# Kernel optimization log

Measured on AMD Instinct MI355X. Metric: run time of the kernel, lower is better.

## Reference

```python
import math
import jax, jax.numpy as jnp
import numpy as np

N_EMBD = 1024
N_HEAD = 16
HEAD_DIM = N_EMBD // N_HEAD


def setup_inputs() -> dict:
    key = jax.random.key(0)
    ks = jax.random.split(key, 5)
    B, S = 4, 2048
    x = jax.random.normal(ks[0], (B, S, 2, N_EMBD), dtype=jnp.float32)
    Wt = jax.random.normal(ks[1], (N_EMBD, 3 * N_EMBD), dtype=jnp.float32) * 0.02
    Ws = jax.random.normal(ks[2], (N_EMBD, 2 * N_EMBD), dtype=jnp.float32) * 0.02
    Wo = jax.random.normal(ks[3], (N_EMBD, N_EMBD), dtype=jnp.float32) * 0.02
    lam_ts = jnp.ones((1,), dtype=jnp.float32)
    lam_st = jnp.ones((1,), dtype=jnp.float32)
    lam_ss = jnp.ones((1,), dtype=jnp.float32)
    return {"x": x, "Wt": Wt, "Ws": Ws, "Wo": Wo,
            "lam_ts": lam_ts, "lam_st": lam_st, "lam_ss": lam_ss}


def _heads(t, B, S):
    # [B,S,E] -> [B,H,S,D]
    return t.reshape(B, S, N_HEAD, HEAD_DIM).transpose(0, 2, 1, 3)


def reference(x, Wt, Ws, Wo, lam_ts, lam_st, lam_ss):
    B, S, _, E = x.shape
    xt = x[:, :, 0, :]  # text stream [B,S,E]
    xs = x[:, :, 1, :]  # spatial stream [B,S,E]

    qt, kt, vt = jnp.split(xt @ Wt, 3, axis=-1)
    qs, ks = jnp.split(xs @ Ws, 2, axis=-1)
    qt, kt, vt = _heads(qt, B, S), _heads(kt, B, S), _heads(vt, B, S)
    qs, ks = _heads(qs, B, S), _heads(ks, B, S)

    scale = 1.0 / math.sqrt(HEAD_DIM)
    att = (jnp.einsum('bhqd,bhkd->bhqk', qt, kt)
           + lam_ts[0] * jnp.einsum('bhqd,bhkd->bhqk', qt, ks)
           + lam_st[0] * jnp.einsum('bhqd,bhkd->bhqk', qs, kt)
           + lam_ss[0] * jnp.einsum('bhqd,bhkd->bhqk', qs, ks)) * scale
    att = jax.nn.softmax(att, axis=-1)

    y = jnp.einsum('bhqk,bhkd->bhqd', att, vt)  # [B,H,S,D]
    y = y.transpose(0, 2, 1, 3).reshape(B, S, E)
    y = y @ Wo
    # concat text output with untouched spatial stream -> [B,S,2,E]
    return jnp.concatenate([y[:, :, None, :], xs[:, :, None, :]], axis=2)
```

## Files before the change

kernel.cpp:

```cpp
#include <hip/hip_runtime.h>

typedef short  short8  __attribute__((ext_vector_type(8)));
typedef float  f32x4   __attribute__((ext_vector_type(4)));
typedef ushort u16x4   __attribute__((ext_vector_type(4)));

__device__ __forceinline__ float bf2f(ushort u) {
  union { unsigned u; float f; } v; v.u = ((unsigned)u) << 16; return v.f;
}
__device__ __forceinline__ ushort f2bf(float f) {
  union { float f; unsigned u; } v; v.f = f;
  unsigned r = v.u + 0x7FFF + ((v.u >> 16) & 1);
  return (ushort)(r >> 16);
}
__device__ __forceinline__ float exp2_fast(float x) {
  float r; asm("v_exp_f32 %0, %1" : "=v"(r) : "v"(x)); return r;
}

__device__ __forceinline__ void gload16(const ushort* g, ushort* l) {
  __builtin_amdgcn_global_load_lds(
      (__attribute__((address_space(1))) void*)(void*)(const_cast<ushort*>(g)),
      (__attribute__((address_space(3))) void*)(void*)l, 16, 0, 0);
}


__global__ __launch_bounds__(256) void prep_x(const float* __restrict__ x,
                                              ushort* __restrict__ xt,
                                              ushort* __restrict__ xs,
                                              float* __restrict__ out) {
  size_t i = ((size_t)blockIdx.x * 256 + threadIdx.x) * 4;
  size_t m = i >> 10, e = i & 1023;
  f32x4 a = *(const f32x4*)&x[m * 2048 + e];
  f32x4 b = *(const f32x4*)&x[m * 2048 + 1024 + e];
  u16x4 ta, tb;
#pragma unroll
  for (int j = 0; j < 4; ++j) { ta[j] = f2bf(a[j]); tb[j] = f2bf(b[j]); }
  *(u16x4*)&xt[i] = ta;
  *(u16x4*)&xs[i] = tb;
  *(f32x4*)&out[m * 2048 + 1024 + e] = b;
}

__global__ __launch_bounds__(256) void transpose_w(const float* __restrict__ W,
                                                   ushort* __restrict__ Wt,
                                                   int K, int N) {
  __shared__ float tile[32][33];
  int n0 = blockIdx.x * 32, k0 = blockIdx.y * 32;
  int tx = threadIdx.x & 31, ty = threadIdx.x >> 5;
#pragma unroll
  for (int i = 0; i < 32; i += 8)
    tile[ty + i][tx] = W[(size_t)(k0 + ty + i) * N + n0 + tx];
  __syncthreads();
#pragma unroll
  for (int i = 0; i < 32; i += 8)
    Wt[(size_t)(n0 + ty + i) * K + k0 + tx] = f2bf(tile[tx][ty + i]);
}

template <int F32OUT>
__global__ __launch_bounds__(256) void gemm_bt(const ushort* __restrict__ A,
                                               const ushort* __restrict__ Bt,
                                               ushort* __restrict__ Cb,
                                               float* __restrict__ Cf,
                                               int N, int ldc) {
  const int K = 1024;
  __shared__ ushort sA[128 * 32];
  __shared__ ushort sB[128 * 32];
  const int tid = threadIdx.x;
  const int wave = tid >> 6, lane = tid & 63;
  const int wr = wave >> 1, wc = wave & 1;
  const int l15 = lane & 15, l4 = lane >> 4;
  const int m0 = blockIdx.y * 128, n0 = blockIdx.x * 128;

  f32x4 acc[4][4];
  const f32x4 z = {0.f, 0.f, 0.f, 0.f};
#pragma unroll
  for (int a = 0; a < 4; ++a)
#pragma unroll
    for (int b = 0; b < 4; ++b) acc[a][b] = z;

  for (int k0 = 0; k0 < K; k0 += 32) {
#pragma unroll
    for (int j = 0; j < 2; ++j) {
      int cb = j * 256 + wave * 64;
      int c = cb + lane;
      int row = c >> 2, cc = c & 3;
      gload16(&A [(size_t)(m0 + row) * K + k0 + cc * 8], &sA[cb * 8]);
      gload16(&Bt[(size_t)(n0 + row) * K + k0 + cc * 8], &sB[cb * 8]);
    }
    __syncthreads();
    short8 af[4], bfr[4];
#pragma unroll
    for (int i = 0; i < 4; ++i) {
      af[i]  = *(const short8*)&sA[(wr * 64 + i * 16 + l15) * 32 + l4 * 8];
      bfr[i] = *(const short8*)&sB[(wc * 64 + i * 16 + l15) * 32 + l4 * 8];
    }
#pragma unroll
    for (int mi = 0; mi < 4; ++mi)
#pragma unroll
      for (int ni = 0; ni < 4; ++ni)
        acc[mi][ni] = __builtin_amdgcn_mfma_f32_16x16x32_bf16(af[mi], bfr[ni], acc[mi][ni], 0, 0, 0);
    __syncthreads();
  }

#pragma unroll
  for (int mi = 0; mi < 4; ++mi)
#pragma unroll
    for (int ni = 0; ni < 4; ++ni) {
      int row = m0 + wr * 64 + mi * 16 + l4 * 4;
      int col = n0 + wc * 64 + ni * 16 + l15;
#pragma unroll
      for (int r = 0; r < 4; ++r) {
        if constexpr (F32OUT) Cf[(size_t)(row + r) * ldc + col] = acc[mi][ni][r];
        else                  Cb[(size_t)(row + r) * ldc + col] = f2bf(acc[mi][ni][r]);
      }
    }
}

__global__ __launch_bounds__(256) void scatter_qk(const ushort* __restrict__ Ct,
                                                  const ushort* __restrict__ Cs,
                                                  ushort* __restrict__ Qb,
                                                  ushort* __restrict__ Kb,
                                                  const float* plts, const float* plst,
                                                  const float* plss) {
  int tid = blockIdx.x * 256 + threadIdx.x;
  int m = tid >> 7, u = tid & 127;
  int b = m >> 11, s = m & 2047;
  int h = u >> 3, din = (u & 7) * 8;
  float lts = plts[0], lst = plst[0], lss = plss[0];
  const float scale = 0.125f * 1.44269504f;
  short8 qt = *(const short8*)&Ct[(size_t)m * 3072 + u * 8];
  short8 kt = *(const short8*)&Ct[(size_t)m * 3072 + 1024 + u * 8];
  short8 qs = *(const short8*)&Cs[(size_t)m * 2048 + u * 8];
  short8 ks = *(const short8*)&Cs[(size_t)m * 2048 + 1024 + u * 8];
  short8 oqt, oqs, k1, k2;
#pragma unroll
  for (int j = 0; j < 8; ++j) {
    float fqt = bf2f((ushort)qt[j]), fqs = bf2f((ushort)qs[j]);
    float fkt = bf2f((ushort)kt[j]), fks = bf2f((ushort)ks[j]);
    oqt[j] = (short)f2bf(fqt * scale);
    oqs[j] = (short)f2bf(fqs * scale);
    k1[j]  = (short)f2bf(fkt + lts * fks);
    k2[j]  = (short)f2bf(lst * fkt + lss * fks);
  }
  size_t base = ((size_t)(b * 16 + h) * 2048 + s) * 128;
  *(short8*)&Qb[base + din]      = oqt;
  *(short8*)&Qb[base + 64 + din] = oqs;
  int c1 = ((u & 7) ^ (s & 7)) * 8;
  *(short8*)&Kb[base + c1]      = k1;
  *(short8*)&Kb[base + 64 + c1] = k2;
}

__global__ __launch_bounds__(256) void transpose_v(const ushort* __restrict__ Ct,
                                                   ushort* __restrict__ Vt) {
  int bh = blockIdx.y; int s0 = blockIdx.x * 64;
  int b = bh >> 4, h = bh & 15;
  __shared__ ushort t[64][72];
  int tid = threadIdx.x;
#pragma unroll
  for (int j = 0; j < 2; ++j) {
    int c = j * 256 + tid;
    int srow = c >> 3, cc = c & 7;
    *(short8*)&t[srow][cc * 8] =
        *(const short8*)&Ct[(size_t)(b * 2048 + s0 + srow) * 3072 + 2048 + h * 64 + cc * 8];
  }
  __syncthreads();
#pragma unroll
  for (int j = 0; j < 2; ++j) {
    int c = j * 256 + tid;
    int drow = c >> 3, cc = c & 7;
    short8 v;
#pragma unroll
    for (int k = 0; k < 8; ++k) v[k] = t[cc * 8 + k][drow];
    *(short8*)&Vt[((size_t)bh * 64 + drow) * 2048 + s0 + ((cc ^ (drow & 7)) * 8)] = v;
  }
}

__global__ __launch_bounds__(256) void attn_kernel(const ushort* __restrict__ Q,
                                                   const ushort* __restrict__ Kg,
                                                   const ushort* __restrict__ Vg,
                                                   ushort* __restrict__ Y) {
  const int id   = blockIdx.x;
  const int virt = (id & 7) * 128 + (id >> 3);
  const int bh = virt >> 4;
  const int q0 = (virt & 15) * 128;
  const int tid = threadIdx.x;
  const int wave = tid >> 6, lane = tid & 63;
  const int l15 = lane & 15, l4 = lane >> 4;
  const size_t qkb = (size_t)bh * 2048 * 128;
  const size_t vb  = (size_t)bh * 64 * 2048;

  __shared__ ushort sKV[2 * 64 * 128 + 2 * 64 * 64];
  ushort* const sK0 = sKV;
  ushort* const sV0 = sKV + 2 * 64 * 128;

  auto stage = [&](int kv0, int bufi) {
    ushort* dK = sK0 + bufi * (64 * 128);
    ushort* dV = sV0 + bufi * (64 * 64);
#pragma unroll
    for (int j = 0; j < 4; ++j) {
      int base = j * 256 + wave * 64;
      int c = base + lane, row = c >> 4, cc = c & 15;
      gload16(&Kg[qkb + (size_t)(kv0 + row) * 128 + cc * 8], &dK[base * 8]);
    }
#pragma unroll
    for (int j = 0; j < 2; ++j) {
      int base = j * 256 + wave * 64;
      int c = base + lane, row = c >> 3, cc = c & 7;
      gload16(&Vg[vb + (size_t)row * 2048 + kv0 + cc * 8], &dV[base * 8]);
    }
  };

  short8 qf[2][4];
#pragma unroll
  for (int qi = 0; qi < 2; ++qi) {
    int qrow = q0 + wave * 32 + qi * 16 + l15;
#pragma unroll
    for (int kk = 0; kk < 4; ++kk)
      qf[qi][kk] = *(const short8*)&Q[qkb + (size_t)qrow * 128 + kk * 32 + l4 * 8];
  }
  const f32x4 z = {0.f, 0.f, 0.f, 0.f};
  f32x4 accO[2][4] = {{z, z, z, z}, {z, z, z, z}};
  float mrow[2] = {-3.0e38f, -3.0e38f}, lrow[2] = {0.f, 0.f};

  stage(0, 0);
  __syncthreads();

  for (int t = 0; t < 32; ++t) {
    const int cur = t & 1;
    if (t < 31) stage((t + 1) * 64, cur ^ 1);
    const ushort* cK = sK0 + cur * (64 * 128);
    const ushort* cV = sV0 + cur * (64 * 64);

    f32x4 sc[2][4] = {{z, z, z, z}, {z, z, z, z}};
    __builtin_amdgcn_s_setprio(1);
#pragma unroll
    for (int kk = 0; kk < 4; ++kk)
#pragma unroll
      for (int kb = 0; kb < 4; ++kb) {
        int row = kb * 16 + l15;
        const short8 kf = *(const short8*)&cK[row * 128 + (((kk * 4 + l4) ^ (row & 7)) * 8)];
        sc[0][kb] = __builtin_amdgcn_mfma_f32_16x16x32_bf16(kf, qf[0][kk], sc[0][kb], 0, 0, 0);
        sc[1][kb] = __builtin_amdgcn_mfma_f32_16x16x32_bf16(kf, qf[1][kk], sc[1][kb], 0, 0, 0);
      }
    __builtin_amdgcn_s_setprio(0);

    union { uint u4[4]; short8 s8; } pa[2][2];
#pragma unroll
    for (int qi = 0; qi < 2; ++qi) {
      float mx = sc[qi][0][0];
#pragma unroll
      for (int kb = 0; kb < 4; ++kb)
#pragma unroll
        for (int r = 0; r < 4; ++r) mx = fmaxf(mx, sc[qi][kb][r]);
      mx = fmaxf(mx, __shfl_xor(mx, 16));
      mx = fmaxf(mx, __shfl_xor(mx, 32));

      if (__any(mx > mrow[qi] + 8.f)) {
        float mnew = fmaxf(mrow[qi], mx);
        float corr = exp2_fast(mrow[qi] - mnew);
        mrow[qi] = mnew;
        lrow[qi] *= corr;
#pragma unroll
        for (int r = 0; r < 4; ++r) {
          float cq = __shfl(corr, l4 * 4 + r);
#pragma unroll
          for (int nf = 0; nf < 4; ++nf) accO[qi][nf][r] *= cq;
        }
      }

      float ps = 0.f;
#pragma unroll
      for (int kb = 0; kb < 4; ++kb)
#pragma unroll
        for (int r = 0; r < 4; ++r) {
          float e = exp2_fast(sc[qi][kb][r] - mrow[qi]);
          sc[qi][kb][r] = e; ps += e;
        }
      lrow[qi] += ps;

      uint u00, u01, u10, u11, u20, u21, u30, u31;
#define CVTPK(d, a, b) asm("v_cvt_pk_bf16_f32 %0, %1, %2" : "=v"(d) : "v"(a), "v"(b))
      CVTPK(u00, sc[qi][0][0], sc[qi][0][1]); CVTPK(u01, sc[qi][0][2], sc[qi][0][3]);
      CVTPK(u10, sc[qi][1][0], sc[qi][1][1]); CVTPK(u11, sc[qi][1][2], sc[qi][1][3]);
      CVTPK(u20, sc[qi][2][0], sc[qi][2][1]); CVTPK(u21, sc[qi][2][2], sc[qi][2][3]);
      CVTPK(u30, sc[qi][3][0], sc[qi][3][1]); CVTPK(u31, sc[qi][3][2], sc[qi][3][3]);
#undef CVTPK
      asm volatile("v_permlane32_swap_b32 %0, %1" : "+v"(u00), "+v"(u10));
      asm volatile("v_permlane32_swap_b32 %0, %1" : "+v"(u01), "+v"(u11));
      asm volatile("v_permlane32_swap_b32 %0, %1" : "+v"(u20), "+v"(u30));
      asm volatile("v_permlane32_swap_b32 %0, %1" : "+v"(u21), "+v"(u31));
      asm volatile("v_permlane16_swap_b32 %0, %1" : "+v"(u00), "+v"(u10));
      asm volatile("v_permlane16_swap_b32 %0, %1" : "+v"(u01), "+v"(u11));
      asm volatile("v_permlane16_swap_b32 %0, %1" : "+v"(u20), "+v"(u30));
      asm volatile("v_permlane16_swap_b32 %0, %1" : "+v"(u21), "+v"(u31));
      pa[qi][0].u4[0] = u00; pa[qi][0].u4[1] = u01; pa[qi][0].u4[2] = u10; pa[qi][0].u4[3] = u11;
      pa[qi][1].u4[0] = u20; pa[qi][1].u4[1] = u21; pa[qi][1].u4[2] = u30; pa[qi][1].u4[3] = u31;
    }

    __builtin_amdgcn_s_setprio(1);
#pragma unroll
    for (int nf = 0; nf < 4; ++nf) {
      int d = nf * 16 + l15;
      const short8 vf0 = *(const short8*)&cV[d * 64 + ((l4 ^ (d & 7)) * 8)];
      const short8 vf1 = *(const short8*)&cV[d * 64 + (((4 + l4) ^ (d & 7)) * 8)];
      accO[0][nf] = __builtin_amdgcn_mfma_f32_16x16x32_bf16(pa[0][0].s8, vf0, accO[0][nf], 0, 0, 0);
      accO[1][nf] = __builtin_amdgcn_mfma_f32_16x16x32_bf16(pa[1][0].s8, vf0, accO[1][nf], 0, 0, 0);
      accO[0][nf] = __builtin_amdgcn_mfma_f32_16x16x32_bf16(pa[0][1].s8, vf1, accO[0][nf], 0, 0, 0);
      accO[1][nf] = __builtin_amdgcn_mfma_f32_16x16x32_bf16(pa[1][1].s8, vf1, accO[1][nf], 0, 0, 0);
    }
    __builtin_amdgcn_s_setprio(0);

    __syncthreads();
  }

  int b = bh >> 4, hh = bh & 15;
#pragma unroll
  for (int qi = 0; qi < 2; ++qi) {
    float ls = lrow[qi] + __shfl_xor(lrow[qi], 16);
    ls += __shfl_xor(ls, 32);
    float linv = 1.f / ls;
#pragma unroll
    for (int r = 0; r < 4; ++r) {
      float lq = __shfl(linv, l4 * 4 + r);
      int q = q0 + wave * 32 + qi * 16 + l4 * 4 + r;
#pragma unroll
      for (int nf = 0; nf < 4; ++nf)
        Y[((size_t)b * 2048 + q) * 1024 + hh * 64 + nf * 16 + l15] =
            f2bf(accO[qi][nf][r] * lq);
    }
  }
}

extern "C" void kernel_launch(void* const* d_in, const int* in_sizes, int n_in,
                              void* d_out, int out_size, void* d_ws, size_t ws_size,
                              hipStream_t stream) {
  const float* x   = (const float*)d_in[0];
  const float* Wt  = (const float*)d_in[1];
  const float* Ws  = (const float*)d_in[2];
  const float* Wo  = (const float*)d_in[3];
  const float* lts = (const float*)d_in[4];
  const float* lst = (const float*)d_in[5];
  const float* lss = (const float*)d_in[6];
  float* out = (float*)d_out;
  char* ws = (char*)d_ws;

  ushort* xt    = (ushort*)(ws + 0);
  ushort* xs    = (ushort*)(ws + 16777216);
  ushort* Qbuf  = (ushort*)(ws + 0);
  ushort* Wt_bt = (ushort*)(ws + 33554432);
  ushort* Ws_bt = (ushort*)(ws + 39845888);
  ushort* Wo_bt = (ushort*)(ws + 44040192);
  ushort* Ct    = (ushort*)(ws + 46137344);
  ushort* Ybuf  = (ushort*)(ws + 46137344);
  ushort* Cs    = (ushort*)(ws + 96468992);
  ushort* Kbuf  = (ushort*)(ws + 130023424);
  ushort* Vtbuf = (ushort*)(ws + 163577856);
  (void)in_sizes; (void)n_in; (void)out_size; (void)ws_size;

  prep_x<<<8192, 256, 0, stream>>>(x, xt, xs, out);
  transpose_w<<<dim3(96, 32), 256, 0, stream>>>(Wt, Wt_bt, 1024, 3072);
  transpose_w<<<dim3(64, 32), 256, 0, stream>>>(Ws, Ws_bt, 1024, 2048);
  transpose_w<<<dim3(32, 32), 256, 0, stream>>>(Wo, Wo_bt, 1024, 1024);
  gemm_bt<0><<<dim3(24, 64), 256, 0, stream>>>(xt, Wt_bt, Ct, nullptr, 3072, 3072);
  gemm_bt<0><<<dim3(16, 64), 256, 0, stream>>>(xs, Ws_bt, Cs, nullptr, 2048, 2048);
  scatter_qk<<<4096, 256, 0, stream>>>(Ct, Cs, Qbuf, Kbuf, lts, lst, lss);
  transpose_v<<<dim3(32, 64), 256, 0, stream>>>(Ct, Vtbuf);
  attn_kernel<<<1024, 256, 0, stream>>>(Qbuf, Kbuf, Vtbuf, Ybuf);
  gemm_bt<1><<<dim3(8, 64), 256, 0, stream>>>(Ybuf, Wo_bt, nullptr, out, 1024, 2048);
}
```

Baseline: 335.4 us.

## Replace double-buffered K/V staging with single buffers and split-phase prefetch

Shared memory for K and V drops from two buffers each to one, which cuts LDS use per block roughly in half and may allow more resident blocks per CU. The next K tile is loaded after the softmax (overlapping the PV MFMAs), and the next V tile after the end-of-iteration barrier. This adds a barrier per iteration and leaves less time to hide load latency, since the next QK step waits on K fetched during PV only.

```diff
diff --git a/kernel.cpp b/kernel.cpp
--- a/kernel.cpp
+++ b/kernel.cpp
@@ -187,24 +187,23 @@
   const size_t qkb = (size_t)bh * 2048 * 128;
   const size_t vb  = (size_t)bh * 64 * 2048;
 
-  __shared__ ushort sKV[2 * 64 * 128 + 2 * 64 * 64];
-  ushort* const sK0 = sKV;
-  ushort* const sV0 = sKV + 2 * 64 * 128;
-
-  auto stage = [&](int kv0, int bufi) {
-    ushort* dK = sK0 + bufi * (64 * 128);
-    ushort* dV = sV0 + bufi * (64 * 64);
+  __shared__ ushort sK[64 * 128];
+  __shared__ ushort sV[64 * 64];
+
+  auto stageK = [&](int kv0) {
 #pragma unroll
     for (int j = 0; j < 4; ++j) {
       int base = j * 256 + wave * 64;
       int c = base + lane, row = c >> 4, cc = c & 15;
-      gload16(&Kg[qkb + (size_t)(kv0 + row) * 128 + cc * 8], &dK[base * 8]);
-    }
+      gload16(&Kg[qkb + (size_t)(kv0 + row) * 128 + cc * 8], &sK[base * 8]);
+    }
+  };
+  auto stageV = [&](int kv0) {
 #pragma unroll
     for (int j = 0; j < 2; ++j) {
       int base = j * 256 + wave * 64;
       int c = base + lane, row = c >> 3, cc = c & 7;
-      gload16(&Vg[vb + (size_t)row * 2048 + kv0 + cc * 8], &dV[base * 8]);
+      gload16(&Vg[vb + (size_t)row * 2048 + kv0 + cc * 8], &sV[base * 8]);
     }
   };
 
@@ -220,15 +219,11 @@
   f32x4 accO[2][4] = {{z, z, z, z}, {z, z, z, z}};
   float mrow[2] = {-3.0e38f, -3.0e38f}, lrow[2] = {0.f, 0.f};
 
-  stage(0, 0);
+  stageK(0);
+  stageV(0);
   __syncthreads();
 
   for (int t = 0; t < 32; ++t) {
-    const int cur = t & 1;
-    if (t < 31) stage((t + 1) * 64, cur ^ 1);
-    const ushort* cK = sK0 + cur * (64 * 128);
-    const ushort* cV = sV0 + cur * (64 * 64);
-
     f32x4 sc[2][4] = {{z, z, z, z}, {z, z, z, z}};
     __builtin_amdgcn_s_setprio(1);
 #pragma unroll
@@ -236,7 +231,7 @@
 #pragma unroll
       for (int kb = 0; kb < 4; ++kb) {
         int row = kb * 16 + l15;
-        const short8 kf = *(const short8*)&cK[row * 128 + (((kk * 4 + l4) ^ (row & 7)) * 8)];
+        const short8 kf = *(const short8*)&sK[row * 128 + (((kk * 4 + l4) ^ (row & 7)) * 8)];
         sc[0][kb] = __builtin_amdgcn_mfma_f32_16x16x32_bf16(kf, qf[0][kk], sc[0][kb], 0, 0, 0);
         sc[1][kb] = __builtin_amdgcn_mfma_f32_16x16x32_bf16(kf, qf[1][kk], sc[1][kb], 0, 0, 0);
       }
@@ -295,12 +290,15 @@
       pa[qi][1].u4[0] = u20; pa[qi][1].u4[1] = u21; pa[qi][1].u4[2] = u30; pa[qi][1].u4[3] = u31;
     }
 
+    __syncthreads();
+    if (t < 31) stageK((t + 1) * 64);
+
     __builtin_amdgcn_s_setprio(1);
 #pragma unroll
     for (int nf = 0; nf < 4; ++nf) {
       int d = nf * 16 + l15;
-      const short8 vf0 = *(const short8*)&cV[d * 64 + ((l4 ^ (d & 7)) * 8)];
-      const short8 vf1 = *(const short8*)&cV[d * 64 + (((4 + l4) ^ (d & 7)) * 8)];
+      const short8 vf0 = *(const short8*)&sV[d * 64 + ((l4 ^ (d & 7)) * 8)];
+      const short8 vf1 = *(const short8*)&sV[d * 64 + (((4 + l4) ^ (d & 7)) * 8)];
       accO[0][nf] = __builtin_amdgcn_mfma_f32_16x16x32_bf16(pa[0][0].s8, vf0, accO[0][nf], 0, 0, 0);
       accO[1][nf] = __builtin_amdgcn_mfma_f32_16x16x32_bf16(pa[1][0].s8, vf0, accO[1][nf], 0, 0, 0);
       accO[0][nf] = __builtin_amdgcn_mfma_f32_16x16x32_bf16(pa[0][1].s8, vf1, accO[0][nf], 0, 0, 0);
@@ -309,6 +307,7 @@
     __builtin_amdgcn_s_setprio(0);
 
     __syncthreads();
+    if (t < 31) stageV((t + 1) * 64);
   }
 
   int b = bh >> 4, hh = bh & 15;
```

Measured after the change: 341.3 us. Within noise of the previous version (+1.8%).

## Fuse Q/K scatter and lambda mixing into projection GEMM epilogues

Applied to the files above, without the earlier changes.

Removes the scatter_qk kernel. The text-stream GEMM now writes Q heads directly into the head-major Q buffer and keeps only K/V in a smaller row-major buffer. The spatial GEMM writes Qs into the buffer and computes the lambda-mixed swizzled K from the stored Kt in its epilogue. The softmax scale on Q is folded into the transposed weights. This saves one kernel launch and a full read/write pass over the Q/K intermediates, but the epilogue now does scalar 2-byte scattered stores instead of vectorized 16-byte ones.

```diff
diff --git a/kernel.cpp b/kernel.cpp
--- a/kernel.cpp
+++ b/kernel.cpp
@@ -41,7 +41,8 @@
 
 __global__ __launch_bounds__(256) void transpose_w(const float* __restrict__ W,
                                                    ushort* __restrict__ Wt,
-                                                   int K, int N) {
+                                                   int K, int N, int nq,
+                                                   float qscale) {
   __shared__ float tile[32][33];
   int n0 = blockIdx.x * 32, k0 = blockIdx.y * 32;
   int tx = threadIdx.x & 31, ty = threadIdx.x >> 5;
@@ -50,16 +51,25 @@
     tile[ty + i][tx] = W[(size_t)(k0 + ty + i) * N + n0 + tx];
   __syncthreads();
 #pragma unroll
-  for (int i = 0; i < 32; i += 8)
-    Wt[(size_t)(n0 + ty + i) * K + k0 + tx] = f2bf(tile[tx][ty + i]);
-}
-
-template <int F32OUT>
+  for (int i = 0; i < 32; i += 8) {
+    int n = n0 + ty + i;
+    float v = tile[tx][ty + i];
+    if (n < nq) v *= qscale;
+    Wt[(size_t)n * K + k0 + tx] = f2bf(v);
+  }
+}
+
+template <int EPI>
 __global__ __launch_bounds__(256) void gemm_bt(const ushort* __restrict__ A,
                                                const ushort* __restrict__ Bt,
-                                               ushort* __restrict__ Cb,
-                                               float* __restrict__ Cf,
-                                               int N, int ldc) {
+                                               int N,
+                                               ushort* __restrict__ o1,
+                                               ushort* __restrict__ o2,
+                                               const ushort* __restrict__ ct2,
+                                               float* __restrict__ of,
+                                               const float* plts,
+                                               const float* plst,
+                                               const float* plss) {
   const int K = 1024;
   __shared__ ushort sA[128 * 32];
   __shared__ ushort sB[128 * 32];
@@ -100,55 +110,60 @@
     __syncthreads();
   }
 
+  float lts = 0.f, lst = 0.f, lss = 0.f;
+  if constexpr (EPI == 2) { lts = plts[0]; lst = plst[0]; lss = plss[0]; }
+
 #pragma unroll
   for (int mi = 0; mi < 4; ++mi)
 #pragma unroll
     for (int ni = 0; ni < 4; ++ni) {
-      int row = m0 + wr * 64 + mi * 16 + l4 * 4;
-      int col = n0 + wc * 64 + ni * 16 + l15;
-#pragma unroll
-      for (int r = 0; r < 4; ++r) {
-        if constexpr (F32OUT) Cf[(size_t)(row + r) * ldc + col] = acc[mi][ni][r];
-        else                  Cb[(size_t)(row + r) * ldc + col] = f2bf(acc[mi][ni][r]);
+      int rowb = m0 + wr * 64 + mi * 16 + l4 * 4;
+      int col  = n0 + wc * 64 + ni * 16 + l15;
+      if constexpr (EPI == 0) {
+#pragma unroll
+        for (int r = 0; r < 4; ++r)
+          of[(size_t)(rowb + r) * 2048 + col] = acc[mi][ni][r];
+      } else if constexpr (EPI == 1) {
+        if (col < 1024) {
+          int h = col >> 6, d = col & 63;
+#pragma unroll
+          for (int r = 0; r < 4; ++r) {
+            int s = rowb + r, b = s >> 11, ss = s & 2047;
+            o1[((size_t)(b * 16 + h) * 2048 + ss) * 128 + d] = f2bf(acc[mi][ni][r]);
+          }
+        } else {
+#pragma unroll
+          for (int r = 0; r < 4; ++r)
+            o2[(size_t)(rowb + r) * 2048 + (col - 1024)] = f2bf(acc[mi][ni][r]);
+        }
+      } else {
+        if (col < 1024) {
+          int h = col >> 6, d = col & 63;
+#pragma unroll
+          for (int r = 0; r < 4; ++r) {
+            int s = rowb + r, b = s >> 11, ss = s & 2047;
+            o1[((size_t)(b * 16 + h) * 2048 + ss) * 128 + 64 + d] = f2bf(acc[mi][ni][r]);
+          }
+        } else {
+          int d64 = col - 1024, h = d64 >> 6, d = d64 & 63;
+#pragma unroll
+          for (int r = 0; r < 4; ++r) {
+            int s = rowb + r, b = s >> 11, ss = s & 2047;
+            float kt = bf2f(ct2[(size_t)s * 2048 + d64]);
+            float ks = acc[mi][ni][r];
+            float k1 = kt + lts * ks;
+            float k2 = lst * kt + lss * ks;
+            size_t base = ((size_t)(b * 16 + h) * 2048 + ss) * 128;
+            int off = ((((d >> 3) ^ (ss & 7)) << 3)) + (d & 7);
+            o2[base + off]      = f2bf(k1);
+            o2[base + 64 + off] = f2bf(k2);
+          }
+        }
       }
     }
 }
 
-__global__ __launch_bounds__(256) void scatter_qk(const ushort* __restrict__ Ct,
-                                                  const ushort* __restrict__ Cs,
-                                                  ushort* __restrict__ Qb,
-                                                  ushort* __restrict__ Kb,
-                                                  const float* plts, const float* plst,
-                                                  const float* plss) {
-  int tid = blockIdx.x * 256 + threadIdx.x;
-  int m = tid >> 7, u = tid & 127;
-  int b = m >> 11, s = m & 2047;
-  int h = u >> 3, din = (u & 7) * 8;
-  float lts = plts[0], lst = plst[0], lss = plss[0];
-  const float scale = 0.125f * 1.44269504f;
-  short8 qt = *(const short8*)&Ct[(size_t)m * 3072 + u * 8];
-  short8 kt = *(const short8*)&Ct[(size_t)m * 3072 + 1024 + u * 8];
-  short8 qs = *(const short8*)&Cs[(size_t)m * 2048 + u * 8];
-  short8 ks = *(const short8*)&Cs[(size_t)m * 2048 + 1024 + u * 8];
-  short8 oqt, oqs, k1, k2;
-#pragma unroll
-  for (int j = 0; j < 8; ++j) {
-    float fqt = bf2f((ushort)qt[j]), fqs = bf2f((ushort)qs[j]);
-    float fkt = bf2f((ushort)kt[j]), fks = bf2f((ushort)ks[j]);
-    oqt[j] = (short)f2bf(fqt * scale);
-    oqs[j] = (short)f2bf(fqs * scale);
-    k1[j]  = (short)f2bf(fkt + lts * fks);
-    k2[j]  = (short)f2bf(lst * fkt + lss * fks);
-  }
-  size_t base = ((size_t)(b * 16 + h) * 2048 + s) * 128;
-  *(short8*)&Qb[base + din]      = oqt;
-  *(short8*)&Qb[base + 64 + din] = oqs;
-  int c1 = ((u & 7) ^ (s & 7)) * 8;
-  *(short8*)&Kb[base + c1]      = k1;
-  *(short8*)&Kb[base + 64 + c1] = k2;
-}
-
-__global__ __launch_bounds__(256) void transpose_v(const ushort* __restrict__ Ct,
+__global__ __launch_bounds__(256) void transpose_v(const ushort* __restrict__ Ct2,
                                                    ushort* __restrict__ Vt) {
   int bh = blockIdx.y; int s0 = blockIdx.x * 64;
   int b = bh >> 4, h = bh & 15;
@@ -159,7 +174,7 @@
     int c = j * 256 + tid;
     int srow = c >> 3, cc = c & 7;
     *(short8*)&t[srow][cc * 8] =
-        *(const short8*)&Ct[(size_t)(b * 2048 + s0 + srow) * 3072 + 2048 + h * 64 + cc * 8];
+        *(const short8*)&Ct2[(size_t)(b * 2048 + s0 + srow) * 2048 + 1024 + h * 64 + cc * 8];
   }
   __syncthreads();
 #pragma unroll
@@ -344,25 +359,28 @@
 
   ushort* xt    = (ushort*)(ws + 0);
   ushort* xs    = (ushort*)(ws + 16777216);
-  ushort* Qbuf  = (ushort*)(ws + 0);
   ushort* Wt_bt = (ushort*)(ws + 33554432);
   ushort* Ws_bt = (ushort*)(ws + 39845888);
   ushort* Wo_bt = (ushort*)(ws + 44040192);
-  ushort* Ct    = (ushort*)(ws + 46137344);
-  ushort* Ybuf  = (ushort*)(ws + 46137344);
-  ushort* Cs    = (ushort*)(ws + 96468992);
-  ushort* Kbuf  = (ushort*)(ws + 130023424);
-  ushort* Vtbuf = (ushort*)(ws + 163577856);
+  ushort* Ct2   = (ushort*)(ws + 46137344);
+  ushort* Qbuf  = (ushort*)(ws + 79691776);
+  ushort* Kbuf  = (ushort*)(ws + 113246208);
+  ushort* Vtbuf = (ushort*)(ws + 146800640);
+  ushort* Ybuf  = (ushort*)(ws + 163577856);
   (void)in_sizes; (void)n_in; (void)out_size; (void)ws_size;
 
+  const float qscale = 0.125f * 1.44269504f;
+
   prep_x<<<8192, 256, 0, stream>>>(x, xt, xs, out);
-  transpose_w<<<dim3(96, 32), 256, 0, stream>>>(Wt, Wt_bt, 1024, 3072);
-  transpose_w<<<dim3(64, 32), 256, 0, stream>>>(Ws, Ws_bt, 1024, 2048);
-  transpose_w<<<dim3(32, 32), 256, 0, stream>>>(Wo, Wo_bt, 1024, 1024);
-  gemm_bt<0><<<dim3(24, 64), 256, 0, stream>>>(xt, Wt_bt, Ct, nullptr, 3072, 3072);
-  gemm_bt<0><<<dim3(16, 64), 256, 0, stream>>>(xs, Ws_bt, Cs, nullptr, 2048, 2048);
-  scatter_qk<<<4096, 256, 0, stream>>>(Ct, Cs, Qbuf, Kbuf, lts, lst, lss);
-  transpose_v<<<dim3(32, 64), 256, 0, stream>>>(Ct, Vtbuf);
+  transpose_w<<<dim3(96, 32), 256, 0, stream>>>(Wt, Wt_bt, 1024, 3072, 1024, qscale);
+  transpose_w<<<dim3(64, 32), 256, 0, stream>>>(Ws, Ws_bt, 1024, 2048, 1024, qscale);
+  transpose_w<<<dim3(32, 32), 256, 0, stream>>>(Wo, Wo_bt, 1024, 1024, 0, 1.f);
+  gemm_bt<1><<<dim3(24, 64), 256, 0, stream>>>(xt, Wt_bt, 3072, Qbuf, Ct2,
+                                               nullptr, nullptr, nullptr, nullptr, nullptr);
+  gemm_bt<2><<<dim3(16, 64), 256, 0, stream>>>(xs, Ws_bt, 2048, Qbuf, Kbuf,
+                                               Ct2, nullptr, lts, lst, lss);
+  transpose_v<<<dim3(32, 64), 256, 0, stream>>>(Ct2, Vtbuf);
   attn_kernel<<<1024, 256, 0, stream>>>(Qbuf, Kbuf, Vtbuf, Ybuf);
-  gemm_bt<1><<<dim3(8, 64), 256, 0, stream>>>(Ybuf, Wo_bt, nullptr, out, 1024, 2048);
-}
+  gemm_bt<0><<<dim3(8, 64), 256, 0, stream>>>(Ybuf, Wo_bt, 1024, nullptr, nullptr,
+                                              nullptr, out, nullptr, nullptr, nullptr);
+}
```

New measurement: 342.8 us. 1.02x slower.
